# Performance work log

Measured on AMD Instinct MI355X. Metric: run time of the kernel, lower is better.

## Reference

```python
import jax, jax.numpy as jnp
import numpy as np

N = 50000      # nodes
E = 800000     # edges
F_IN = 128     # input node feature dim
H = 4          # attention heads
DH = 64        # per-head hidden dim
HID = H * DH   # 256
NEG_SLOPE = 0.2


def gat_conv(h, src, dst, W, al, ar, b, res):
    # DGL GATConv: project, compute attention logits, edge softmax over dst, aggregate.
    feat = (h @ W).reshape(N, H, DH)                      # [N,H,DH]
    el = jnp.einsum('nhd,hd->nh', feat, al)               # [N,H]
    er = jnp.einsum('nhd,hd->nh', feat, ar)               # [N,H]
    e = el[src] + er[dst]                                 # [E,H]
    e = jnp.where(e > 0, e, NEG_SLOPE * e)                # LeakyReLU(0.2)
    m = jax.ops.segment_max(e, dst, num_segments=N)       # [N,H]
    m = jnp.where(jnp.isfinite(m), m, 0.0)                # zero-in-degree safety
    ex = jnp.exp(e - m[dst])                              # [E,H]
    denom = jax.ops.segment_sum(ex, dst, num_segments=N)  # [N,H]
    alpha = ex / jnp.maximum(denom[dst], 1e-16)           # edge softmax
    out = jax.ops.segment_sum(feat[src] * alpha[:, :, None], dst, num_segments=N)
    return out + res.reshape(N, H, DH) + b.reshape(1, H, DH)


def setup_inputs() -> dict:
    key = jax.random.key(0)
    ks = jax.random.split(key, 16)
    x = jax.random.normal(ks[0], (N, F_IN), jnp.float32)
    edge_index = jax.random.randint(ks[1], (2, E), 0, N)
    s_in = 1.0 / np.sqrt(F_IN)
    s_h = 1.0 / np.sqrt(HID)
    W0 = jax.random.normal(ks[2], (F_IN, HID), jnp.float32) * s_in
    W1 = jax.random.normal(ks[3], (HID, HID), jnp.float32) * s_h
    W2 = jax.random.normal(ks[4], (HID, HID), jnp.float32) * s_h
    al0 = jax.random.normal(ks[5], (H, DH), jnp.float32) * 0.1
    al1 = jax.random.normal(ks[6], (H, DH), jnp.float32) * 0.1
    al2 = jax.random.normal(ks[7], (H, DH), jnp.float32) * 0.1
    ar0 = jax.random.normal(ks[8], (H, DH), jnp.float32) * 0.1
    ar1 = jax.random.normal(ks[9], (H, DH), jnp.float32) * 0.1
    ar2 = jax.random.normal(ks[10], (H, DH), jnp.float32) * 0.1
    b0 = jnp.zeros((HID,), jnp.float32)
    b1 = jnp.zeros((HID,), jnp.float32)
    b2 = jnp.zeros((HID,), jnp.float32)
    resW0 = jax.random.normal(ks[11], (F_IN, HID), jnp.float32) * s_in
    return {"x": x, "edge_index": edge_index,
            "W0": W0, "W1": W1, "W2": W2,
            "al0": al0, "al1": al1, "al2": al2,
            "ar0": ar0, "ar1": ar1, "ar2": ar2,
            "b0": b0, "b1": b1, "b2": b2,
            "resW0": resW0}


def reference(x, edge_index, W0, W1, W2, al0, al1, al2, ar0, ar1, ar2, b0, b1, b2, resW0):
    src, dst = edge_index[0], edge_index[1]
    # layer 0: residual via linear projection (in != heads*hidden)
    h = gat_conv(x, src, dst, W0, al0, ar0, b0, x @ resW0).reshape(N, HID)
    h = jax.nn.relu(h)
    # layer 1: identity residual
    h = gat_conv(h, src, dst, W1, al1, ar1, b1, h).reshape(N, HID)
    h = jax.nn.relu(h)
    # layer 2: identity residual, mean over heads
    h = gat_conv(h, src, dst, W2, al2, ar2, b2, h)
    return h.mean(axis=1)  # [N, DH]
```

## Files before the change

kernel.cpp:

```cpp
#include <hip/hip_runtime.h>
#include <math.h>

#define N_NODES 50000
#define N_EDGES 800000
#define F_INPUT 128
#define HEADS 4
#define DHID 64
#define HID 256
#define M_PAD 50048
#define SCAN_B 49

typedef _Float16 half8 __attribute__((ext_vector_type(8)));
typedef _Float16 half4 __attribute__((ext_vector_type(4)));
typedef float f32x4 __attribute__((ext_vector_type(4)));


__global__ void hist_kernel(const int* __restrict__ dst, int* __restrict__ counts) {
    int e = blockIdx.x * 256 + threadIdx.x;
    if (e < N_EDGES) atomicAdd(&counts[dst[e]], 1);
}

__global__ __launch_bounds__(256) void scan1_kernel(const int* __restrict__ counts,
                                                    int* __restrict__ pre,
                                                    int* __restrict__ bsum) {
    __shared__ int buf[256];
    int tid = threadIdx.x;
    int idx = blockIdx.x * 1024 + tid * 4;
    int v0 = 0, v1 = 0, v2 = 0, v3 = 0;
    if (idx + 3 < N_NODES) {
        int4 v = *(const int4*)&counts[idx];
        v0 = v.x; v1 = v.y; v2 = v.z; v3 = v.w;
    } else {
        if (idx + 0 < N_NODES) v0 = counts[idx + 0];
        if (idx + 1 < N_NODES) v1 = counts[idx + 1];
        if (idx + 2 < N_NODES) v2 = counts[idx + 2];
    }
    int s0 = v0, s1 = s0 + v1, s2 = s1 + v2, s3 = s2 + v3;
    buf[tid] = s3;
    __syncthreads();
    for (int off = 1; off < 256; off <<= 1) {
        int t = (tid >= off) ? buf[tid - off] : 0;
        __syncthreads();
        buf[tid] += t;
        __syncthreads();
    }
    int excl = buf[tid] - s3;
    if (idx + 0 < N_NODES) pre[idx + 0] = excl + s0;
    if (idx + 1 < N_NODES) pre[idx + 1] = excl + s1;
    if (idx + 2 < N_NODES) pre[idx + 2] = excl + s2;
    if (idx + 3 < N_NODES) pre[idx + 3] = excl + s3;
    if (tid == 255) bsum[blockIdx.x] = buf[255];
}

__global__ void scan2_kernel(const int* __restrict__ bsum, int* __restrict__ bpre) {
    int lane = threadIdx.x;
    int v = (lane < SCAN_B) ? bsum[lane] : 0;
    int orig = v;
#pragma unroll
    for (int off = 1; off < 64; off <<= 1) {
        int t = __shfl_up(v, off, 64);
        if (lane >= off) v += t;
    }
    if (lane < SCAN_B) bpre[lane] = v - orig;
}

__global__ __launch_bounds__(256) void scan3_kernel(const int* __restrict__ pre,
                                                    const int* __restrict__ bpre,
                                                    int* __restrict__ row_ptr) {
    int add = bpre[blockIdx.x];
    int idx = blockIdx.x * 1024 + threadIdx.x * 4;
#pragma unroll
    for (int u = 0; u < 4; u++) {
        int i = idx + u;
        if (i < N_NODES) row_ptr[i + 1] = pre[i] + add;
    }
    if (blockIdx.x == 0 && threadIdx.x == 0) row_ptr[0] = 0;
}

__global__ void scatter_kernel(const int* __restrict__ src, const int* __restrict__ dst,
                               const int* __restrict__ row_ptr, int* __restrict__ cursor,
                               int* __restrict__ esrc) {
    int e = blockIdx.x * 256 + threadIdx.x;
    if (e < N_EDGES) {
        int d = dst[e];
        int pos = row_ptr[d] + atomicAdd(&cursor[d], 1);
        esrc[pos] = src[e];
    }
}


__global__ void cvt_x_kernel(const float* __restrict__ x, _Float16* __restrict__ x16) {
    int t = blockIdx.x * 256 + threadIdx.x;
    if (t < N_NODES * F_INPUT / 4) {
        f32x4 v = *(const f32x4*)&x[t * 4];
        half4 h = {(_Float16)v.x, (_Float16)v.y, (_Float16)v.z, (_Float16)v.w};
        *(half4*)&x16[(size_t)t * 4] = h;
    }
}

__global__ void wt_all_kernel(const float* __restrict__ W0, const float* __restrict__ WR,
                              _Float16* __restrict__ WtL0,
                              const float* __restrict__ W1, _Float16* __restrict__ Wt1,
                              const float* __restrict__ W2, _Float16* __restrict__ Wt2) {
    int t = blockIdx.x * 256 + threadIdx.x;
    if (t < 65536) {
        int c = t >> 7;
        int k = t & 127;
        float v = (c < 256) ? W0[k * 256 + c] : WR[k * 256 + (c - 256)];
        WtL0[t] = (_Float16)v;
    } else if (t < 131072) {
        int u = t - 65536;
        int c = u >> 8;
        int k = u & 255;
        Wt1[u] = (_Float16)W1[k * 256 + c];
    } else if (t < 196608) {
        int u = t - 131072;
        int c = u >> 8;
        int k = u & 255;
        Wt2[u] = (_Float16)W2[k * 256 + c];
    }
}

__global__ void wlwr_kernel(const float* __restrict__ W0, const float* __restrict__ al0,
                            const float* __restrict__ ar0, _Float16* __restrict__ WtL0,
                            const float* __restrict__ W1, const float* __restrict__ al1,
                            const float* __restrict__ ar1, _Float16* __restrict__ Wt1,
                            const float* __restrict__ W2, const float* __restrict__ al2,
                            const float* __restrict__ ar2, _Float16* __restrict__ Wt2) {
    int t = blockIdx.x * 256 + threadIdx.x;
    if (t < 2048) {
        int row8 = t >> 7, k = t & 127;
        float v = 0.f;
        if (row8 < 8) {
            int h = row8 & 3;
            const float* vec = (row8 < 4) ? al0 : ar0;
            float s = 0.f;
            for (int d = 0; d < 64; d++) s += W0[k * 256 + h * 64 + d] * vec[h * 64 + d];
            v = s;
        }
        WtL0[(512 + row8) * 128 + k] = (_Float16)v;
    } else if (t < 6144) {
        int u = t - 2048;
        int row8 = u >> 8, k = u & 255;
        float v = 0.f;
        if (row8 < 8) {
            int h = row8 & 3;
            const float* vec = (row8 < 4) ? al1 : ar1;
            float s = 0.f;
            for (int d = 0; d < 64; d++) s += W1[k * 256 + h * 64 + d] * vec[h * 64 + d];
            v = s;
        }
        Wt1[(256 + row8) * 256 + k] = (_Float16)v;
    } else if (t < 10240) {
        int u = t - 6144;
        int row8 = u >> 8, k = u & 255;
        float v = 0.f;
        if (row8 < 8) {
            int h = row8 & 3;
            const float* vec = (row8 < 4) ? al2 : ar2;
            float s = 0.f;
            for (int d = 0; d < 64; d++) s += W2[k * 256 + h * 64 + d] * vec[h * 64 + d];
            v = s;
        }
        Wt2[(256 + row8) * 256 + k] = (_Float16)v;
    }
}


__device__ __forceinline__ void gl2lds16(const void* g, void* l) {
    __builtin_amdgcn_global_load_lds((const __attribute__((address_space(1))) void*)g,
                                     (__attribute__((address_space(3))) void*)l, 16, 0, 0);
}

__global__ __launch_bounds__(512) void gemm_l0(const _Float16* __restrict__ A16,
                                               const _Float16* __restrict__ WtL0,
                                               _Float16* __restrict__ feat16,
                                               _Float16* __restrict__ res16,
                                               float* __restrict__ el, float* __restrict__ er) {
    __shared__ __align__(16) _Float16 As[4 * 512];
    __shared__ __align__(16) _Float16 Ws[33 * 512];
    int tid = threadIdx.x;
    int w = tid >> 6;
    int lane = tid & 63;
    int lrow = lane & 15;
    int lk = lane >> 4;
    int row0 = blockIdx.x * 64;

    f32x4 acc[4][4] = {};
    f32x4 acc5[4] = {};

    for (int k0 = 0; k0 < F_INPUT; k0 += 32) {
        if (w < 4)
            gl2lds16(A16 + (size_t)(row0 + w * 16 + lrow) * F_INPUT + k0 + lk * 8, &As[w * 512]);
#pragma unroll
        for (int i = 0; i < 4; i++) {
            int tt = i * 8 + w;
            gl2lds16(WtL0 + (size_t)(tt * 16 + lrow) * F_INPUT + k0 + lk * 8, &Ws[tt * 512]);
        }
        if (w == 7)
            gl2lds16(WtL0 + (size_t)(512 + lrow) * F_INPUT + k0 + lk * 8, &Ws[32 * 512]);
        __syncthreads();
        half8 a[4], b[4], b5;
#pragma unroll
        for (int m = 0; m < 4; m++) a[m] = *(const half8*)&As[m * 512 + lane * 8];
#pragma unroll
        for (int j = 0; j < 4; j++) b[j] = *(const half8*)&Ws[(w * 4 + j) * 512 + lane * 8];
        if (w == 3) b5 = *(const half8*)&Ws[32 * 512 + lane * 8];
#pragma unroll
        for (int m = 0; m < 4; m++)
#pragma unroll
            for (int j = 0; j < 4; j++)
                acc[m][j] = __builtin_amdgcn_mfma_f32_16x16x32_f16(a[m], b[j], acc[m][j], 0, 0, 0);
        if (w == 3) {
#pragma unroll
            for (int m = 0; m < 4; m++)
                acc5[m] = __builtin_amdgcn_mfma_f32_16x16x32_f16(a[m], b5, acc5[m], 0, 0, 0);
        }
        __syncthreads();
    }

    if (w < 4) {
#pragma unroll
        for (int m = 0; m < 4; m++) {
#pragma unroll
            for (int r = 0; r < 4; r++) {
                int row = row0 + m * 16 + lk * 4 + r;
                if (row < N_NODES) {
#pragma unroll
                    for (int j = 0; j < 4; j++)
                        feat16[(size_t)row * HID + w * 64 + j * 16 + lrow] = (_Float16)acc[m][j][r];
                }
            }
        }
        if (w == 3 && lrow < 8) {
#pragma unroll
            for (int m = 0; m < 4; m++) {
#pragma unroll
                for (int r = 0; r < 4; r++) {
                    int row = row0 + m * 16 + lk * 4 + r;
                    if (row < N_NODES) {
                        float v = acc5[m][r];
                        if (lrow < 4) el[row * 4 + lrow] = v;
                        else          er[row * 4 + (lrow - 4)] = v;
                    }
                }
            }
        }
    } else {
        int wc = w - 4;
#pragma unroll
        for (int m = 0; m < 4; m++) {
#pragma unroll
            for (int r = 0; r < 4; r++) {
                int row = row0 + m * 16 + lk * 4 + r;
                if (row < N_NODES) {
#pragma unroll
                    for (int j = 0; j < 4; j++)
                        res16[(size_t)row * HID + wc * 64 + j * 16 + lrow] = (_Float16)acc[m][j][r];
                }
            }
        }
    }
}

__global__ __launch_bounds__(512) void gemm_h(const _Float16* __restrict__ A16,
                                              const _Float16* __restrict__ Wt,
                                              _Float16* __restrict__ feat16,
                                              float* __restrict__ el, float* __restrict__ er) {
    __shared__ __align__(16) _Float16 As[8 * 512];
    __shared__ __align__(16) _Float16 Ws[17 * 512];
    int tid = threadIdx.x;
    int w = tid >> 6;
    int lane = tid & 63;
    int lrow = lane & 15;
    int lk = lane >> 4;
    int wrow = w >> 2;
    int wcol = w & 3;
    int row0 = blockIdx.x * 128;

    f32x4 acc[4][4] = {};
    f32x4 acc5[4] = {};

    for (int k0 = 0; k0 < HID; k0 += 32) {
        gl2lds16(A16 + (size_t)(row0 + w * 16 + lrow) * HID + k0 + lk * 8, &As[w * 512]);
        gl2lds16(Wt + (size_t)(w * 16 + lrow) * HID + k0 + lk * 8, &Ws[w * 512]);
        gl2lds16(Wt + (size_t)((w + 8) * 16 + lrow) * HID + k0 + lk * 8, &Ws[(w + 8) * 512]);
        if (w == 0)
            gl2lds16(Wt + (size_t)(256 + lrow) * HID + k0 + lk * 8, &Ws[16 * 512]);
        __syncthreads();
        half8 a[4], b[4], b5;
#pragma unroll
        for (int m = 0; m < 4; m++) a[m] = *(const half8*)&As[(wrow * 4 + m) * 512 + lane * 8];
#pragma unroll
        for (int j = 0; j < 4; j++) b[j] = *(const half8*)&Ws[(wcol * 4 + j) * 512 + lane * 8];
        if (wcol == 3) b5 = *(const half8*)&Ws[16 * 512 + lane * 8];
#pragma unroll
        for (int m = 0; m < 4; m++)
#pragma unroll
            for (int j = 0; j < 4; j++)
                acc[m][j] = __builtin_amdgcn_mfma_f32_16x16x32_f16(a[m], b[j], acc[m][j], 0, 0, 0);
        if (wcol == 3) {
#pragma unroll
            for (int m = 0; m < 4; m++)
                acc5[m] = __builtin_amdgcn_mfma_f32_16x16x32_f16(a[m], b5, acc5[m], 0, 0, 0);
        }
        __syncthreads();
    }

#pragma unroll
    for (int m = 0; m < 4; m++) {
#pragma unroll
        for (int r = 0; r < 4; r++) {
            int row = row0 + wrow * 64 + m * 16 + lk * 4 + r;
            if (row < N_NODES) {
#pragma unroll
                for (int j = 0; j < 4; j++)
                    feat16[(size_t)row * HID + wcol * 64 + j * 16 + lrow] = (_Float16)acc[m][j][r];
            }
        }
    }
    if (wcol == 3 && lrow < 8) {
#pragma unroll
        for (int m = 0; m < 4; m++) {
#pragma unroll
            for (int r = 0; r < 4; r++) {
                int row = row0 + wrow * 64 + m * 16 + lk * 4 + r;
                if (row < N_NODES) {
                    float v = acc5[m][r];
                    if (lrow < 4) el[row * 4 + lrow] = v;
                    else          er[row * 4 + (lrow - 4)] = v;
                }
            }
        }
    }
}


__global__ __launch_bounds__(256) void agg_kernel(const _Float16* __restrict__ feat16,
                                                  const float* __restrict__ el,
                                                  const float* __restrict__ er,
                                                  const int* __restrict__ row_ptr,
                                                  const int* __restrict__ esrc,
                                                  const _Float16* __restrict__ res16,
                                                  const float* __restrict__ bias,
                                                  _Float16* __restrict__ out16,
                                                  float* __restrict__ outmean,
                                                  int do_relu) {
    __shared__ float lds[4][4 * 65 + 64];
    int wv = threadIdx.x >> 6;
    int lane = threadIdx.x & 63;
    int n = blockIdx.x * 4 + wv;
    int li = lane & 31;
    int sub = lane >> 5;
    int head = li >> 3;
    int start = row_ptr[n];
    int deg = row_ptr[n + 1] - start;
    f32x4 ern = *(const f32x4*)&er[n * 4];
    float* L = lds[wv];
    float* Loff = L + 4 * 65;
    const float* Lex = L + head * 65;

    f32x4 accA = {0.f, 0.f, 0.f, 0.f};
    f32x4 accB = {0.f, 0.f, 0.f, 0.f};
    f32x4 sm4 = {0.f, 0.f, 0.f, 0.f};
    const char* fbase = (const char*)feat16 + li * 16;

    for (int base = 0; base < deg; base += 64) {
        int e = base + lane;
        f32x4 ex4 = {0.f, 0.f, 0.f, 0.f};
        int off = 0;
        if (e < deg) {
            int s = esrc[start + e];
            off = s * (HID * 2);
            f32x4 v = *(const f32x4*)&el[s * 4];
            v = v + ern;
            v.x = v.x > 0.f ? v.x : 0.2f * v.x;
            v.y = v.y > 0.f ? v.y : 0.2f * v.y;
            v.z = v.z > 0.f ? v.z : 0.2f * v.z;
            v.w = v.w > 0.f ? v.w : 0.2f * v.w;
            ex4.x = __expf(v.x);
            ex4.y = __expf(v.y);
            ex4.z = __expf(v.z);
            ex4.w = __expf(v.w);
        }
        L[0 * 65 + lane] = ex4.x;
        L[1 * 65 + lane] = ex4.y;
        L[2 * 65 + lane] = ex4.z;
        L[3 * 65 + lane] = ex4.w;
        Loff[lane] = __int_as_float(off);
        sm4 += ex4;

        int cnt = min(64, deg - base);
        int cnt16 = (cnt + 15) & ~15;
        for (int j = 0; j < cnt16; j += 16) {
            float ex[8]; int o[8];
#pragma unroll
            for (int u = 0; u < 8; u++) {
                int e2 = j + u * 2 + sub;
                ex[u] = Lex[e2];
                o[u] = __float_as_int(Loff[e2]);
            }
            half8 f[8];
#pragma unroll
            for (int u = 0; u < 8; u++) f[u] = *(const half8*)(fbase + o[u]);
#pragma unroll
            for (int u = 0; u < 8; u++) {
                accA.x += ex[u] * (float)f[u][0];
                accA.y += ex[u] * (float)f[u][1];
                accA.z += ex[u] * (float)f[u][2];
                accA.w += ex[u] * (float)f[u][3];
                accB.x += ex[u] * (float)f[u][4];
                accB.y += ex[u] * (float)f[u][5];
                accB.z += ex[u] * (float)f[u][6];
                accB.w += ex[u] * (float)f[u][7];
            }
        }
    }

    accA.x += __shfl_xor(accA.x, 32, 64);
    accA.y += __shfl_xor(accA.y, 32, 64);
    accA.z += __shfl_xor(accA.z, 32, 64);
    accA.w += __shfl_xor(accA.w, 32, 64);
    accB.x += __shfl_xor(accB.x, 32, 64);
    accB.y += __shfl_xor(accB.y, 32, 64);
    accB.z += __shfl_xor(accB.z, 32, 64);
    accB.w += __shfl_xor(accB.w, 32, 64);

#pragma unroll
    for (int off2 = 1; off2 < 64; off2 <<= 1) {
        sm4.x += __shfl_xor(sm4.x, off2, 64);
        sm4.y += __shfl_xor(sm4.y, off2, 64);
        sm4.z += __shfl_xor(sm4.z, off2, 64);
        sm4.w += __shfl_xor(sm4.w, off2, 64);
    }
    float smh = (head == 0) ? sm4.x : (head == 1) ? sm4.y : (head == 2) ? sm4.z : sm4.w;
    float inv = 1.f / fmaxf(smh, 1e-16f);
    accA *= inv;
    accB *= inv;

    half8 rv = *(const half8*)&res16[(size_t)n * HID + li * 8];
    f32x4 bvA = *(const f32x4*)&bias[li * 8];
    f32x4 bvB = *(const f32x4*)&bias[li * 8 + 4];
    accA.x += (float)rv[0] + bvA.x;
    accA.y += (float)rv[1] + bvA.y;
    accA.z += (float)rv[2] + bvA.z;
    accA.w += (float)rv[3] + bvA.w;
    accB.x += (float)rv[4] + bvB.x;
    accB.y += (float)rv[5] + bvB.y;
    accB.z += (float)rv[6] + bvB.z;
    accB.w += (float)rv[7] + bvB.w;
    if (do_relu) {
        accA.x = fmaxf(accA.x, 0.f); accA.y = fmaxf(accA.y, 0.f);
        accA.z = fmaxf(accA.z, 0.f); accA.w = fmaxf(accA.w, 0.f);
        accB.x = fmaxf(accB.x, 0.f); accB.y = fmaxf(accB.y, 0.f);
        accB.z = fmaxf(accB.z, 0.f); accB.w = fmaxf(accB.w, 0.f);
    }
    if (outmean) {
#pragma unroll
        for (int st = 8; st <= 16; st <<= 1) {
            accA.x += __shfl_xor(accA.x, st, 64);
            accA.y += __shfl_xor(accA.y, st, 64);
            accA.z += __shfl_xor(accA.z, st, 64);
            accA.w += __shfl_xor(accA.w, st, 64);
            accB.x += __shfl_xor(accB.x, st, 64);
            accB.y += __shfl_xor(accB.y, st, 64);
            accB.z += __shfl_xor(accB.z, st, 64);
            accB.w += __shfl_xor(accB.w, st, 64);
        }
        if (sub == 0 && li < 8) {
            f32x4 moA = accA * 0.25f;
            f32x4 moB = accB * 0.25f;
            *(f32x4*)&outmean[(size_t)n * DHID + li * 8] = moA;
            *(f32x4*)&outmean[(size_t)n * DHID + li * 8 + 4] = moB;
        }
    } else {
        if (sub == 0) {
            half8 h = {(_Float16)accA.x, (_Float16)accA.y, (_Float16)accA.z, (_Float16)accA.w,
                       (_Float16)accB.x, (_Float16)accB.y, (_Float16)accB.z, (_Float16)accB.w};
            *(half8*)&out16[(size_t)n * HID + li * 8] = h;
        }
    }
}


extern "C" void kernel_launch(void* const* d_in, const int* in_sizes, int n_in,
                              void* d_out, int out_size, void* d_ws, size_t ws_size,
                              hipStream_t stream) {
    const float* x     = (const float*)d_in[0];
    const int*   ei    = (const int*)d_in[1];
    const float* W0    = (const float*)d_in[2];
    const float* W1    = (const float*)d_in[3];
    const float* W2    = (const float*)d_in[4];
    const float* al0   = (const float*)d_in[5];
    const float* al1   = (const float*)d_in[6];
    const float* al2   = (const float*)d_in[7];
    const float* ar0   = (const float*)d_in[8];
    const float* ar1   = (const float*)d_in[9];
    const float* ar2   = (const float*)d_in[10];
    const float* b0    = (const float*)d_in[11];
    const float* b1    = (const float*)d_in[12];
    const float* b2    = (const float*)d_in[13];
    const float* resW0 = (const float*)d_in[14];
    float* out = (float*)d_out;

    const int* srcp = ei;
    const int* dstp = ei + N_EDGES;

    char* p = (char*)d_ws;
    auto alloc = [&](size_t bytes) -> char* {
        char* r = p;
        p += (bytes + 255) & ~(size_t)255;
        return r;
    };
    _Float16*  h16    = (_Float16*)alloc((size_t)M_PAD * HID * 2);
    _Float16*  feat16 = (_Float16*)alloc((size_t)M_PAD * HID * 2);
    _Float16*  res0   = (_Float16*)alloc((size_t)N_NODES * HID * 2);
    _Float16*  x16    = (_Float16*)alloc((size_t)M_PAD * F_INPUT * 2);
    float*     el     = (float*)alloc((size_t)N_NODES * HEADS * 4);
    float*     er     = (float*)alloc((size_t)N_NODES * HEADS * 4);
    _Float16*  WtL0   = (_Float16*)alloc((size_t)528 * F_INPUT * 2);
    _Float16*  Wt1    = (_Float16*)alloc((size_t)272 * HID * 2);
    _Float16*  Wt2    = (_Float16*)alloc((size_t)272 * HID * 2);
    int*       counts = (int*)alloc((size_t)2 * N_NODES * 4);
    int*       cursor = counts + N_NODES;
    int*       rowptr = (int*)alloc((size_t)(N_NODES + 1) * 4);
    int*       esrc   = (int*)alloc((size_t)N_EDGES * 4);
    int*       pre    = (int*)alloc((size_t)N_NODES * 4);
    int*       bsum   = (int*)alloc((size_t)SCAN_B * 4);
    int*       bpre   = (int*)alloc((size_t)SCAN_B * 4);

    const int EB = (N_EDGES + 255) / 256;
    const int NB = N_NODES / 4;

    hipMemsetAsync(counts, 0, (size_t)2 * N_NODES * 4, stream);
    hist_kernel<<<EB, 256, 0, stream>>>(dstp, counts);
    scan1_kernel<<<SCAN_B, 256, 0, stream>>>(counts, pre, bsum);
    scan2_kernel<<<1, 64, 0, stream>>>(bsum, bpre);
    scan3_kernel<<<SCAN_B, 256, 0, stream>>>(pre, bpre, rowptr);
    scatter_kernel<<<EB, 256, 0, stream>>>(srcp, dstp, rowptr, cursor, esrc);

    cvt_x_kernel<<<(N_NODES * F_INPUT / 4 + 255) / 256, 256, 0, stream>>>(x, x16);
    wt_all_kernel<<<768, 256, 0, stream>>>(W0, resW0, WtL0, W1, Wt1, W2, Wt2);
    wlwr_kernel<<<40, 256, 0, stream>>>(W0, al0, ar0, WtL0, W1, al1, ar1, Wt1, W2, al2, ar2, Wt2);

    gemm_l0<<<M_PAD / 64, 512, 0, stream>>>(x16, WtL0, feat16, res0, el, er);
    agg_kernel<<<NB, 256, 0, stream>>>(feat16, el, er, rowptr, esrc, res0, b0, h16, nullptr, 1);

    gemm_h<<<M_PAD / 128, 512, 0, stream>>>(h16, Wt1, feat16, el, er);
    agg_kernel<<<NB, 256, 0, stream>>>(feat16, el, er, rowptr, esrc, h16, b1, h16, nullptr, 1);

    gemm_h<<<M_PAD / 128, 512, 0, stream>>>(h16, Wt2, feat16, el, er);
    agg_kernel<<<NB, 256, 0, stream>>>(feat16, el, er, rowptr, esrc, h16, b2, nullptr, out, 0);
}
```

Baseline: 492.4 us.

## Fuse prep kernels, add online-max softmax, packed fp16 FMA, 8-wave agg blocks

```diff
diff --git a/kernel.cpp b/kernel.cpp
--- a/kernel.cpp
+++ b/kernel.cpp
@@ -12,6 +12,7 @@
 
 typedef _Float16 half8 __attribute__((ext_vector_type(8)));
 typedef _Float16 half4 __attribute__((ext_vector_type(4)));
+typedef _Float16 half2t __attribute__((ext_vector_type(2)));
 typedef float f32x4 __attribute__((ext_vector_type(4)));
 
 
@@ -89,80 +90,67 @@
 }
 
 
-__global__ void cvt_x_kernel(const float* __restrict__ x, _Float16* __restrict__ x16) {
+#define PREP_A 1600000
+#define PREP_B (PREP_A + 196608)
+#define PREP_C (PREP_B + 10240)
+
+__global__ void prep_kernel(const float* __restrict__ x, _Float16* __restrict__ x16,
+                            const float* __restrict__ W0, const float* __restrict__ WR,
+                            _Float16* __restrict__ WtL0,
+                            const float* __restrict__ W1, _Float16* __restrict__ Wt1,
+                            const float* __restrict__ W2, _Float16* __restrict__ Wt2,
+                            const float* __restrict__ al0, const float* __restrict__ ar0,
+                            const float* __restrict__ al1, const float* __restrict__ ar1,
+                            const float* __restrict__ al2, const float* __restrict__ ar2) {
     int t = blockIdx.x * 256 + threadIdx.x;
-    if (t < N_NODES * F_INPUT / 4) {
+    if (t < PREP_A) {
         f32x4 v = *(const f32x4*)&x[t * 4];
         half4 h = {(_Float16)v.x, (_Float16)v.y, (_Float16)v.z, (_Float16)v.w};
         *(half4*)&x16[(size_t)t * 4] = h;
-    }
-}
-
-__global__ void wt_all_kernel(const float* __restrict__ W0, const float* __restrict__ WR,
-                              _Float16* __restrict__ WtL0,
-                              const float* __restrict__ W1, _Float16* __restrict__ Wt1,
-                              const float* __restrict__ W2, _Float16* __restrict__ Wt2) {
-    int t = blockIdx.x * 256 + threadIdx.x;
-    if (t < 65536) {
-        int c = t >> 7;
-        int k = t & 127;
-        float v = (c < 256) ? W0[k * 256 + c] : WR[k * 256 + (c - 256)];
-        WtL0[t] = (_Float16)v;
-    } else if (t < 131072) {
-        int u = t - 65536;
-        int c = u >> 8;
-        int k = u & 255;
-        Wt1[u] = (_Float16)W1[k * 256 + c];
-    } else if (t < 196608) {
-        int u = t - 131072;
-        int c = u >> 8;
-        int k = u & 255;
-        Wt2[u] = (_Float16)W2[k * 256 + c];
-    }
-}
-
-__global__ void wlwr_kernel(const float* __restrict__ W0, const float* __restrict__ al0,
-                            const float* __restrict__ ar0, _Float16* __restrict__ WtL0,
-                            const float* __restrict__ W1, const float* __restrict__ al1,
-                            const float* __restrict__ ar1, _Float16* __restrict__ Wt1,
-                            const float* __restrict__ W2, const float* __restrict__ al2,
-                            const float* __restrict__ ar2, _Float16* __restrict__ Wt2) {
-    int t = blockIdx.x * 256 + threadIdx.x;
-    if (t < 2048) {
-        int row8 = t >> 7, k = t & 127;
-        float v = 0.f;
-        if (row8 < 8) {
+    } else if (t < PREP_B) {
+        int u = t - PREP_A;
+        if (u < 65536) {
+            int c = u >> 7;
+            int k = u & 127;
+            float v = (c < 256) ? W0[k * 256 + c] : WR[k * 256 + (c - 256)];
+            WtL0[u] = (_Float16)v;
+        } else if (u < 131072) {
+            int w = u - 65536;
+            int c = w >> 8;
+            int k = w & 255;
+            Wt1[w] = (_Float16)W1[k * 256 + c];
+        } else {
+            int w = u - 131072;
+            int c = w >> 8;
+            int k = w & 255;
+            Wt2[w] = (_Float16)W2[k * 256 + c];
+        }
+    } else if (t < PREP_C) {
+        int u = t - PREP_B;
+        if (u < 2048) {
+            int row8 = u >> 7, k = u & 127;
             int h = row8 & 3;
             const float* vec = (row8 < 4) ? al0 : ar0;
             float s = 0.f;
             for (int d = 0; d < 64; d++) s += W0[k * 256 + h * 64 + d] * vec[h * 64 + d];
-            v = s;
-        }
-        WtL0[(512 + row8) * 128 + k] = (_Float16)v;
-    } else if (t < 6144) {
-        int u = t - 2048;
-        int row8 = u >> 8, k = u & 255;
-        float v = 0.f;
-        if (row8 < 8) {
+            WtL0[(512 + row8) * 128 + k] = (_Float16)s;
+        } else if (u < 6144) {
+            int w = u - 2048;
+            int row8 = w >> 8, k = w & 255;
             int h = row8 & 3;
             const float* vec = (row8 < 4) ? al1 : ar1;
             float s = 0.f;
             for (int d = 0; d < 64; d++) s += W1[k * 256 + h * 64 + d] * vec[h * 64 + d];
-            v = s;
-        }
-        Wt1[(256 + row8) * 256 + k] = (_Float16)v;
-    } else if (t < 10240) {
-        int u = t - 6144;
-        int row8 = u >> 8, k = u & 255;
-        float v = 0.f;
-        if (row8 < 8) {
+            Wt1[(256 + row8) * 256 + k] = (_Float16)s;
+        } else {
+            int w = u - 6144;
+            int row8 = w >> 8, k = w & 255;
             int h = row8 & 3;
             const float* vec = (row8 < 4) ? al2 : ar2;
             float s = 0.f;
             for (int d = 0; d < 64; d++) s += W2[k * 256 + h * 64 + d] * vec[h * 64 + d];
-            v = s;
-        }
-        Wt2[(256 + row8) * 256 + k] = (_Float16)v;
+            Wt2[(256 + row8) * 256 + k] = (_Float16)s;
+        }
     }
 }
 
@@ -336,7 +324,7 @@
 }
 
 
-__global__ __launch_bounds__(256) void agg_kernel(const _Float16* __restrict__ feat16,
+__global__ __launch_bounds__(512) void agg_kernel(const _Float16* __restrict__ feat16,
                                                   const float* __restrict__ el,
                                                   const float* __restrict__ er,
                                                   const int* __restrict__ row_ptr,
@@ -346,10 +334,10 @@
                                                   _Float16* __restrict__ out16,
                                                   float* __restrict__ outmean,
                                                   int do_relu) {
-    __shared__ float lds[4][4 * 65 + 64];
+    __shared__ float lds[8][4 * 65 + 64];
     int wv = threadIdx.x >> 6;
     int lane = threadIdx.x & 63;
-    int n = blockIdx.x * 4 + wv;
+    int n = blockIdx.x * 8 + wv;
     int li = lane & 31;
     int sub = lane >> 5;
     int head = li >> 3;
@@ -363,58 +351,91 @@
     f32x4 accA = {0.f, 0.f, 0.f, 0.f};
     f32x4 accB = {0.f, 0.f, 0.f, 0.f};
     f32x4 sm4 = {0.f, 0.f, 0.f, 0.f};
+    f32x4 mx = {-1e30f, -1e30f, -1e30f, -1e30f};
     const char* fbase = (const char*)feat16 + li * 16;
 
     for (int base = 0; base < deg; base += 64) {
         int e = base + lane;
-        f32x4 ex4 = {0.f, 0.f, 0.f, 0.f};
+        f32x4 x = {-1e30f, -1e30f, -1e30f, -1e30f};
         int off = 0;
         if (e < deg) {
             int s = esrc[start + e];
             off = s * (HID * 2);
             f32x4 v = *(const f32x4*)&el[s * 4];
             v = v + ern;
-            v.x = v.x > 0.f ? v.x : 0.2f * v.x;
-            v.y = v.y > 0.f ? v.y : 0.2f * v.y;
-            v.z = v.z > 0.f ? v.z : 0.2f * v.z;
-            v.w = v.w > 0.f ? v.w : 0.2f * v.w;
-            ex4.x = __expf(v.x);
-            ex4.y = __expf(v.y);
-            ex4.z = __expf(v.z);
-            ex4.w = __expf(v.w);
-        }
-        L[0 * 65 + lane] = ex4.x;
-        L[1 * 65 + lane] = ex4.y;
-        L[2 * 65 + lane] = ex4.z;
-        L[3 * 65 + lane] = ex4.w;
+            x.x = v.x > 0.f ? v.x : 0.2f * v.x;
+            x.y = v.y > 0.f ? v.y : 0.2f * v.y;
+            x.z = v.z > 0.f ? v.z : 0.2f * v.z;
+            x.w = v.w > 0.f ? v.w : 0.2f * v.w;
+        }
+        f32x4 cm = x;
+#pragma unroll
+        for (int o2 = 1; o2 < 64; o2 <<= 1) {
+            cm.x = fmaxf(cm.x, __shfl_xor(cm.x, o2, 64));
+            cm.y = fmaxf(cm.y, __shfl_xor(cm.y, o2, 64));
+            cm.z = fmaxf(cm.z, __shfl_xor(cm.z, o2, 64));
+            cm.w = fmaxf(cm.w, __shfl_xor(cm.w, o2, 64));
+        }
+        f32x4 nmx;
+        nmx.x = fmaxf(mx.x, cm.x);
+        nmx.y = fmaxf(mx.y, cm.y);
+        nmx.z = fmaxf(mx.z, cm.z);
+        nmx.w = fmaxf(mx.w, cm.w);
+        f32x4 scl;
+        scl.x = __expf(mx.x - nmx.x);
+        scl.y = __expf(mx.y - nmx.y);
+        scl.z = __expf(mx.z - nmx.z);
+        scl.w = __expf(mx.w - nmx.w);
+        sm4 *= scl;
+        float sclh = (head == 0) ? scl.x : (head == 1) ? scl.y : (head == 2) ? scl.z : scl.w;
+        accA *= sclh;
+        accB *= sclh;
+        f32x4 ex4;
+        ex4.x = __expf(x.x - nmx.x);
+        ex4.y = __expf(x.y - nmx.y);
+        ex4.z = __expf(x.z - nmx.z);
+        ex4.w = __expf(x.w - nmx.w);
+        sm4 += ex4;
+        {
+            unsigned short h0 = __builtin_bit_cast(unsigned short, (_Float16)ex4.x);
+            unsigned short h1 = __builtin_bit_cast(unsigned short, (_Float16)ex4.y);
+            unsigned short h2 = __builtin_bit_cast(unsigned short, (_Float16)ex4.z);
+            unsigned short h3 = __builtin_bit_cast(unsigned short, (_Float16)ex4.w);
+            L[0 * 65 + lane] = __uint_as_float((unsigned)h0 | ((unsigned)h0 << 16));
+            L[1 * 65 + lane] = __uint_as_float((unsigned)h1 | ((unsigned)h1 << 16));
+            L[2 * 65 + lane] = __uint_as_float((unsigned)h2 | ((unsigned)h2 << 16));
+            L[3 * 65 + lane] = __uint_as_float((unsigned)h3 | ((unsigned)h3 << 16));
+        }
         Loff[lane] = __int_as_float(off);
-        sm4 += ex4;
+        mx = nmx;
 
         int cnt = min(64, deg - base);
         int cnt16 = (cnt + 15) & ~15;
+        half2t ha0 = {0, 0}, ha1 = {0, 0}, ha2 = {0, 0}, ha3 = {0, 0};
         for (int j = 0; j < cnt16; j += 16) {
-            float ex[8]; int o[8];
+            float exf[8]; int o[8];
 #pragma unroll
             for (int u = 0; u < 8; u++) {
                 int e2 = j + u * 2 + sub;
-                ex[u] = Lex[e2];
+                exf[u] = Lex[e2];
                 o[u] = __float_as_int(Loff[e2]);
             }
-            half8 f[8];
-#pragma unroll
-            for (int u = 0; u < 8; u++) f[u] = *(const half8*)(fbase + o[u]);
+            uint4 fv[8];
+#pragma unroll
+            for (int u = 0; u < 8; u++) fv[u] = *(const uint4*)(fbase + o[u]);
 #pragma unroll
             for (int u = 0; u < 8; u++) {
-                accA.x += ex[u] * (float)f[u][0];
-                accA.y += ex[u] * (float)f[u][1];
-                accA.z += ex[u] * (float)f[u][2];
-                accA.w += ex[u] * (float)f[u][3];
-                accB.x += ex[u] * (float)f[u][4];
-                accB.y += ex[u] * (float)f[u][5];
-                accB.z += ex[u] * (float)f[u][6];
-                accB.w += ex[u] * (float)f[u][7];
-            }
-        }
+                half2t eh = __builtin_bit_cast(half2t, __float_as_uint(exf[u]));
+                ha0 += eh * __builtin_bit_cast(half2t, fv[u].x);
+                ha1 += eh * __builtin_bit_cast(half2t, fv[u].y);
+                ha2 += eh * __builtin_bit_cast(half2t, fv[u].z);
+                ha3 += eh * __builtin_bit_cast(half2t, fv[u].w);
+            }
+        }
+        accA.x += (float)ha0.x; accA.y += (float)ha0.y;
+        accA.z += (float)ha1.x; accA.w += (float)ha1.y;
+        accB.x += (float)ha2.x; accB.y += (float)ha2.y;
+        accB.z += (float)ha3.x; accB.w += (float)ha3.y;
     }
 
     accA.x += __shfl_xor(accA.x, 32, 64);
@@ -427,11 +448,11 @@
     accB.w += __shfl_xor(accB.w, 32, 64);
 
 #pragma unroll
-    for (int off2 = 1; off2 < 64; off2 <<= 1) {
-        sm4.x += __shfl_xor(sm4.x, off2, 64);
-        sm4.y += __shfl_xor(sm4.y, off2, 64);
-        sm4.z += __shfl_xor(sm4.z, off2, 64);
-        sm4.w += __shfl_xor(sm4.w, off2, 64);
+    for (int o2 = 1; o2 < 64; o2 <<= 1) {
+        sm4.x += __shfl_xor(sm4.x, o2, 64);
+        sm4.y += __shfl_xor(sm4.y, o2, 64);
+        sm4.z += __shfl_xor(sm4.z, o2, 64);
+        sm4.w += __shfl_xor(sm4.w, o2, 64);
     }
     float smh = (head == 0) ? sm4.x : (head == 1) ? sm4.y : (head == 2) ? sm4.z : sm4.w;
     float inv = 1.f / fmaxf(smh, 1e-16f);
@@ -530,7 +551,7 @@
     int*       bpre   = (int*)alloc((size_t)SCAN_B * 4);
 
     const int EB = (N_EDGES + 255) / 256;
-    const int NB = N_NODES / 4;
+    const int NB = N_NODES / 8;
 
     hipMemsetAsync(counts, 0, (size_t)2 * N_NODES * 4, stream);
     hist_kernel<<<EB, 256, 0, stream>>>(dstp, counts);
@@ -539,16 +560,16 @@
     scan3_kernel<<<SCAN_B, 256, 0, stream>>>(pre, bpre, rowptr);
     scatter_kernel<<<EB, 256, 0, stream>>>(srcp, dstp, rowptr, cursor, esrc);
 
-    cvt_x_kernel<<<(N_NODES * F_INPUT / 4 + 255) / 256, 256, 0, stream>>>(x, x16);
-    wt_all_kernel<<<768, 256, 0, stream>>>(W0, resW0, WtL0, W1, Wt1, W2, Wt2);
-    wlwr_kernel<<<40, 256, 0, stream>>>(W0, al0, ar0, WtL0, W1, al1, ar1, Wt1, W2, al2, ar2, Wt2);
+    prep_kernel<<<(PREP_C + 255) / 256, 256, 0, stream>>>(
+        x, x16, W0, resW0, WtL0, W1, Wt1, W2, Wt2,
+        al0, ar0, al1, ar1, al2, ar2);
 
     gemm_l0<<<M_PAD / 64, 512, 0, stream>>>(x16, WtL0, feat16, res0, el, er);
-    agg_kernel<<<NB, 256, 0, stream>>>(feat16, el, er, rowptr, esrc, res0, b0, h16, nullptr, 1);
+    agg_kernel<<<NB, 512, 0, stream>>>(feat16, el, er, rowptr, esrc, res0, b0, h16, nullptr, 1);
 
     gemm_h<<<M_PAD / 128, 512, 0, stream>>>(h16, Wt1, feat16, el, er);
-    agg_kernel<<<NB, 256, 0, stream>>>(feat16, el, er, rowptr, esrc, h16, b1, h16, nullptr, 1);
+    agg_kernel<<<NB, 512, 0, stream>>>(feat16, el, er, rowptr, esrc, h16, b1, h16, nullptr, 1);
 
     gemm_h<<<M_PAD / 128, 512, 0, stream>>>(h16, Wt2, feat16, el, er);
-    agg_kernel<<<NB, 256, 0, stream>>>(feat16, el, er, rowptr, esrc, h16, b2, nullptr, out, 0);
-}
+    agg_kernel<<<NB, 512, 0, stream>>>(feat16, el, er, rowptr, esrc, h16, b2, nullptr, out, 0);
+}
```

Result: slower. 503.9 us (+2.3%).

## Fuse preprocessing kernels, merge scan passes, and deepen GEMM K-step

Applied to the files above, without the earlier changes.

```diff
diff --git a/kernel.cpp b/kernel.cpp
--- a/kernel.cpp
+++ b/kernel.cpp
@@ -15,10 +15,78 @@
 typedef float f32x4 __attribute__((ext_vector_type(4)));
 
 
-__global__ void hist_kernel(const int* __restrict__ dst, int* __restrict__ counts) {
-    int e = blockIdx.x * 256 + threadIdx.x;
-    if (e < N_EDGES) atomicAdd(&counts[dst[e]], 1);
-}
+#define EB_BLOCKS ((N_EDGES + 255) / 256)
+#define PREP_A 1600000
+#define PREP_B (PREP_A + 196608)
+#define PREP_C (PREP_B + 10240)
+#define PB_BLOCKS ((PREP_C + 255) / 256)
+
+__global__ void hist_prep_kernel(const int* __restrict__ dst, int* __restrict__ counts,
+                                 const float* __restrict__ x, _Float16* __restrict__ x16,
+                                 const float* __restrict__ W0, const float* __restrict__ WR,
+                                 _Float16* __restrict__ WtL0,
+                                 const float* __restrict__ W1, _Float16* __restrict__ Wt1,
+                                 const float* __restrict__ W2, _Float16* __restrict__ Wt2,
+                                 const float* __restrict__ al0, const float* __restrict__ ar0,
+                                 const float* __restrict__ al1, const float* __restrict__ ar1,
+                                 const float* __restrict__ al2, const float* __restrict__ ar2) {
+    if (blockIdx.x < EB_BLOCKS) {
+        int e = blockIdx.x * 256 + threadIdx.x;
+        if (e < N_EDGES) atomicAdd(&counts[dst[e]], 1);
+        return;
+    }
+    int t = (blockIdx.x - EB_BLOCKS) * 256 + threadIdx.x;
+    if (t < PREP_A) {
+        f32x4 v = *(const f32x4*)&x[t * 4];
+        half4 h = {(_Float16)v.x, (_Float16)v.y, (_Float16)v.z, (_Float16)v.w};
+        *(half4*)&x16[(size_t)t * 4] = h;
+    } else if (t < PREP_B) {
+        int u = t - PREP_A;
+        if (u < 65536) {
+            int c = u >> 7;
+            int k = u & 127;
+            float v = (c < 256) ? W0[k * 256 + c] : WR[k * 256 + (c - 256)];
+            WtL0[u] = (_Float16)v;
+        } else if (u < 131072) {
+            int w = u - 65536;
+            int c = w >> 8;
+            int k = w & 255;
+            Wt1[w] = (_Float16)W1[k * 256 + c];
+        } else {
+            int w = u - 131072;
+            int c = w >> 8;
+            int k = w & 255;
+            Wt2[w] = (_Float16)W2[k * 256 + c];
+        }
+    } else if (t < PREP_C) {
+        int u = t - PREP_B;
+        if (u < 2048) {
+            int row8 = u >> 7, k = u & 127;
+            int h = row8 & 3;
+            const float* vec = (row8 < 4) ? al0 : ar0;
+            float s = 0.f;
+            for (int d = 0; d < 64; d++) s += W0[k * 256 + h * 64 + d] * vec[h * 64 + d];
+            WtL0[(512 + row8) * 128 + k] = (_Float16)s;
+        } else if (u < 6144) {
+            int w = u - 2048;
+            int row8 = w >> 8, k = w & 255;
+            int h = row8 & 3;
+            const float* vec = (row8 < 4) ? al1 : ar1;
+            float s = 0.f;
+            for (int d = 0; d < 64; d++) s += W1[k * 256 + h * 64 + d] * vec[h * 64 + d];
+            Wt1[(256 + row8) * 256 + k] = (_Float16)s;
+        } else {
+            int w = u - 6144;
+            int row8 = w >> 8, k = w & 255;
+            int h = row8 & 3;
+            const float* vec = (row8 < 4) ? al2 : ar2;
+            float s = 0.f;
+            for (int d = 0; d < 64; d++) s += W2[k * 256 + h * 64 + d] * vec[h * 64 + d];
+            Wt2[(256 + row8) * 256 + k] = (_Float16)s;
+        }
+    }
+}
+
 
 __global__ __launch_bounds__(256) void scan1_kernel(const int* __restrict__ counts,
                                                     int* __restrict__ pre,
@@ -52,29 +120,30 @@
     if (tid == 255) bsum[blockIdx.x] = buf[255];
 }
 
-__global__ void scan2_kernel(const int* __restrict__ bsum, int* __restrict__ bpre) {
-    int lane = threadIdx.x;
-    int v = (lane < SCAN_B) ? bsum[lane] : 0;
-    int orig = v;
-#pragma unroll
-    for (int off = 1; off < 64; off <<= 1) {
-        int t = __shfl_up(v, off, 64);
-        if (lane >= off) v += t;
-    }
-    if (lane < SCAN_B) bpre[lane] = v - orig;
-}
-
-__global__ __launch_bounds__(256) void scan3_kernel(const int* __restrict__ pre,
-                                                    const int* __restrict__ bpre,
-                                                    int* __restrict__ row_ptr) {
-    int add = bpre[blockIdx.x];
-    int idx = blockIdx.x * 1024 + threadIdx.x * 4;
+__global__ __launch_bounds__(256) void scan23_kernel(const int* __restrict__ pre,
+                                                     const int* __restrict__ bsum,
+                                                     int* __restrict__ row_ptr) {
+    __shared__ int bq[64];
+    int tid = threadIdx.x;
+    if (tid < 64) {
+        int v = (tid < SCAN_B) ? bsum[tid] : 0;
+        int orig = v;
+#pragma unroll
+        for (int off = 1; off < 64; off <<= 1) {
+            int t = __shfl_up(v, off, 64);
+            if (tid >= off) v += t;
+        }
+        bq[tid] = v - orig;
+    }
+    __syncthreads();
+    int add = bq[blockIdx.x];
+    int idx = blockIdx.x * 1024 + tid * 4;
 #pragma unroll
     for (int u = 0; u < 4; u++) {
         int i = idx + u;
         if (i < N_NODES) row_ptr[i + 1] = pre[i] + add;
     }
-    if (blockIdx.x == 0 && threadIdx.x == 0) row_ptr[0] = 0;
+    if (blockIdx.x == 0 && tid == 0) row_ptr[0] = 0;
 }
 
 __global__ void scatter_kernel(const int* __restrict__ src, const int* __restrict__ dst,
@@ -85,84 +154,6 @@
         int d = dst[e];
         int pos = row_ptr[d] + atomicAdd(&cursor[d], 1);
         esrc[pos] = src[e];
-    }
-}
-
-
-__global__ void cvt_x_kernel(const float* __restrict__ x, _Float16* __restrict__ x16) {
-    int t = blockIdx.x * 256 + threadIdx.x;
-    if (t < N_NODES * F_INPUT / 4) {
-        f32x4 v = *(const f32x4*)&x[t * 4];
-        half4 h = {(_Float16)v.x, (_Float16)v.y, (_Float16)v.z, (_Float16)v.w};
-        *(half4*)&x16[(size_t)t * 4] = h;
-    }
-}
-
-__global__ void wt_all_kernel(const float* __restrict__ W0, const float* __restrict__ WR,
-                              _Float16* __restrict__ WtL0,
-                              const float* __restrict__ W1, _Float16* __restrict__ Wt1,
-                              const float* __restrict__ W2, _Float16* __restrict__ Wt2) {
-    int t = blockIdx.x * 256 + threadIdx.x;
-    if (t < 65536) {
-        int c = t >> 7;
-        int k = t & 127;
-        float v = (c < 256) ? W0[k * 256 + c] : WR[k * 256 + (c - 256)];
-        WtL0[t] = (_Float16)v;
-    } else if (t < 131072) {
-        int u = t - 65536;
-        int c = u >> 8;
-        int k = u & 255;
-        Wt1[u] = (_Float16)W1[k * 256 + c];
-    } else if (t < 196608) {
-        int u = t - 131072;
-        int c = u >> 8;
-        int k = u & 255;
-        Wt2[u] = (_Float16)W2[k * 256 + c];
-    }
-}
-
-__global__ void wlwr_kernel(const float* __restrict__ W0, const float* __restrict__ al0,
-                            const float* __restrict__ ar0, _Float16* __restrict__ WtL0,
-                            const float* __restrict__ W1, const float* __restrict__ al1,
-                            const float* __restrict__ ar1, _Float16* __restrict__ Wt1,
-                            const float* __restrict__ W2, const float* __restrict__ al2,
-                            const float* __restrict__ ar2, _Float16* __restrict__ Wt2) {
-    int t = blockIdx.x * 256 + threadIdx.x;
-    if (t < 2048) {
-        int row8 = t >> 7, k = t & 127;
-        float v = 0.f;
-        if (row8 < 8) {
-            int h = row8 & 3;
-            const float* vec = (row8 < 4) ? al0 : ar0;
-            float s = 0.f;
-            for (int d = 0; d < 64; d++) s += W0[k * 256 + h * 64 + d] * vec[h * 64 + d];
-            v = s;
-        }
-        WtL0[(512 + row8) * 128 + k] = (_Float16)v;
-    } else if (t < 6144) {
-        int u = t - 2048;
-        int row8 = u >> 8, k = u & 255;
-        float v = 0.f;
-        if (row8 < 8) {
-            int h = row8 & 3;
-            const float* vec = (row8 < 4) ? al1 : ar1;
-            float s = 0.f;
-            for (int d = 0; d < 64; d++) s += W1[k * 256 + h * 64 + d] * vec[h * 64 + d];
-            v = s;
-        }
-        Wt1[(256 + row8) * 256 + k] = (_Float16)v;
-    } else if (t < 10240) {
-        int u = t - 6144;
-        int row8 = u >> 8, k = u & 255;
-        float v = 0.f;
-        if (row8 < 8) {
-            int h = row8 & 3;
-            const float* vec = (row8 < 4) ? al2 : ar2;
-            float s = 0.f;
-            for (int d = 0; d < 64; d++) s += W2[k * 256 + h * 64 + d] * vec[h * 64 + d];
-            v = s;
-        }
-        Wt2[(256 + row8) * 256 + k] = (_Float16)v;
     }
 }
 
@@ -267,8 +258,8 @@
                                               const _Float16* __restrict__ Wt,
                                               _Float16* __restrict__ feat16,
                                               float* __restrict__ el, float* __restrict__ er) {
-    __shared__ __align__(16) _Float16 As[8 * 512];
-    __shared__ __align__(16) _Float16 Ws[17 * 512];
+    __shared__ __align__(16) _Float16 As[8 * 2 * 512];
+    __shared__ __align__(16) _Float16 Ws[17 * 2 * 512];
     int tid = threadIdx.x;
     int w = tid >> 6;
     int lane = tid & 63;
@@ -281,28 +272,37 @@
     f32x4 acc[4][4] = {};
     f32x4 acc5[4] = {};
 
-    for (int k0 = 0; k0 < HID; k0 += 32) {
-        gl2lds16(A16 + (size_t)(row0 + w * 16 + lrow) * HID + k0 + lk * 8, &As[w * 512]);
-        gl2lds16(Wt + (size_t)(w * 16 + lrow) * HID + k0 + lk * 8, &Ws[w * 512]);
-        gl2lds16(Wt + (size_t)((w + 8) * 16 + lrow) * HID + k0 + lk * 8, &Ws[(w + 8) * 512]);
-        if (w == 0)
-            gl2lds16(Wt + (size_t)(256 + lrow) * HID + k0 + lk * 8, &Ws[16 * 512]);
+    for (int k0 = 0; k0 < HID; k0 += 64) {
+#pragma unroll
+        for (int c = 0; c < 2; c++) {
+            int kk = k0 + c * 32 + lk * 8;
+            gl2lds16(A16 + (size_t)(row0 + w * 16 + lrow) * HID + kk, &As[(w * 2 + c) * 512]);
+            gl2lds16(Wt + (size_t)(w * 16 + lrow) * HID + kk, &Ws[(w * 2 + c) * 512]);
+            gl2lds16(Wt + (size_t)((w + 8) * 16 + lrow) * HID + kk, &Ws[((w + 8) * 2 + c) * 512]);
+            if (w == 0)
+                gl2lds16(Wt + (size_t)(256 + lrow) * HID + kk, &Ws[(16 * 2 + c) * 512]);
+        }
         __syncthreads();
-        half8 a[4], b[4], b5;
-#pragma unroll
-        for (int m = 0; m < 4; m++) a[m] = *(const half8*)&As[(wrow * 4 + m) * 512 + lane * 8];
-#pragma unroll
-        for (int j = 0; j < 4; j++) b[j] = *(const half8*)&Ws[(wcol * 4 + j) * 512 + lane * 8];
-        if (wcol == 3) b5 = *(const half8*)&Ws[16 * 512 + lane * 8];
-#pragma unroll
-        for (int m = 0; m < 4; m++)
+#pragma unroll
+        for (int c = 0; c < 2; c++) {
+            half8 a[4], b[4], b5;
+#pragma unroll
+            for (int m = 0; m < 4; m++)
+                a[m] = *(const half8*)&As[((wrow * 4 + m) * 2 + c) * 512 + lane * 8];
 #pragma unroll
             for (int j = 0; j < 4; j++)
-                acc[m][j] = __builtin_amdgcn_mfma_f32_16x16x32_f16(a[m], b[j], acc[m][j], 0, 0, 0);
-        if (wcol == 3) {
+                b[j] = *(const half8*)&Ws[((wcol * 4 + j) * 2 + c) * 512 + lane * 8];
+            if (wcol == 3) b5 = *(const half8*)&Ws[(16 * 2 + c) * 512 + lane * 8];
 #pragma unroll
             for (int m = 0; m < 4; m++)
-                acc5[m] = __builtin_amdgcn_mfma_f32_16x16x32_f16(a[m], b5, acc5[m], 0, 0, 0);
+#pragma unroll
+                for (int j = 0; j < 4; j++)
+                    acc[m][j] = __builtin_amdgcn_mfma_f32_16x16x32_f16(a[m], b[j], acc[m][j], 0, 0, 0);
+            if (wcol == 3) {
+#pragma unroll
+                for (int m = 0; m < 4; m++)
+                    acc5[m] = __builtin_amdgcn_mfma_f32_16x16x32_f16(a[m], b5, acc5[m], 0, 0, 0);
+            }
         }
         __syncthreads();
     }
@@ -527,21 +527,16 @@
     int*       esrc   = (int*)alloc((size_t)N_EDGES * 4);
     int*       pre    = (int*)alloc((size_t)N_NODES * 4);
     int*       bsum   = (int*)alloc((size_t)SCAN_B * 4);
-    int*       bpre   = (int*)alloc((size_t)SCAN_B * 4);
-
-    const int EB = (N_EDGES + 255) / 256;
+
     const int NB = N_NODES / 4;
 
     hipMemsetAsync(counts, 0, (size_t)2 * N_NODES * 4, stream);
-    hist_kernel<<<EB, 256, 0, stream>>>(dstp, counts);
+    hist_prep_kernel<<<EB_BLOCKS + PB_BLOCKS, 256, 0, stream>>>(
+        dstp, counts, x, x16, W0, resW0, WtL0, W1, Wt1, W2, Wt2,
+        al0, ar0, al1, ar1, al2, ar2);
     scan1_kernel<<<SCAN_B, 256, 0, stream>>>(counts, pre, bsum);
-    scan2_kernel<<<1, 64, 0, stream>>>(bsum, bpre);
-    scan3_kernel<<<SCAN_B, 256, 0, stream>>>(pre, bpre, rowptr);
-    scatter_kernel<<<EB, 256, 0, stream>>>(srcp, dstp, rowptr, cursor, esrc);
-
-    cvt_x_kernel<<<(N_NODES * F_INPUT / 4 + 255) / 256, 256, 0, stream>>>(x, x16);
-    wt_all_kernel<<<768, 256, 0, stream>>>(W0, resW0, WtL0, W1, Wt1, W2, Wt2);
-    wlwr_kernel<<<40, 256, 0, stream>>>(W0, al0, ar0, WtL0, W1, al1, ar1, Wt1, W2, al2, ar2, Wt2);
+    scan23_kernel<<<SCAN_B, 256, 0, stream>>>(pre, bsum, rowptr);
+    scatter_kernel<<<EB_BLOCKS, 256, 0, stream>>>(srcp, dstp, rowptr, cursor, esrc);
 
     gemm_l0<<<M_PAD / 64, 512, 0, stream>>>(x16, WtL0, feat16, res0, el, er);
     agg_kernel<<<NB, 256, 0, stream>>>(feat16, el, er, rowptr, esrc, res0, b0, h16, nullptr, 1);
```

Measured after the change: 480.3 us. 2.5% less time.
